# Kernel optimization log

Measured on AMD Instinct MI355X. Metric: run time of the kernel, lower is better.

## Reference

```python
import jax, jax.numpy as jnp
import numpy as np

L, B, T, H = 4, 64, 256, 1024  # layers, batch, seq_len, hidden (=input=output size)


def setup_inputs() -> dict:
    key = jax.random.key(0)
    ks = jax.random.split(key, 5)
    s = 0.03  # ~1/sqrt(H) init scale to avoid gate saturation
    return {
        "x": jax.random.normal(ks[0], (B, T, H), dtype=jnp.float32),
        "W_ih": jax.random.normal(ks[1], (L, 4 * H, H), dtype=jnp.float32) * s,
        "W_hh": jax.random.normal(ks[2], (L, 4 * H, H), dtype=jnp.float32) * s,
        "b_ih": jax.random.normal(ks[3], (L, 4 * H), dtype=jnp.float32) * s,
        "b_hh": jax.random.normal(ks[4], (L, 4 * H), dtype=jnp.float32) * s,
    }


def _lstm_cell(xt, h, c, Wi, Wh, bi, bh):
    # PyTorch LSTMCell: gates = x W_ih^T + b_ih + h W_hh^T + b_hh; order i,f,g,o
    gates = xt @ Wi.T + bi + h @ Wh.T + bh  # [B, 4H]
    i, f, g, o = jnp.split(gates, 4, axis=-1)
    c_new = jax.nn.sigmoid(f) * c + jax.nn.sigmoid(i) * jnp.tanh(g)
    h_new = jax.nn.sigmoid(o) * jnp.tanh(c_new)
    return h_new, c_new


def reference(x, W_ih, W_hh, b_ih, b_hh):
    nlayers, bsz, hid = W_ih.shape[0], x.shape[0], W_hh.shape[-1]
    h0 = jnp.zeros((nlayers, bsz, hid), dtype=x.dtype)
    c0 = jnp.zeros((nlayers, bsz, hid), dtype=x.dtype)

    def step(carry, xt):  # xt: [B, H]
        h, c = carry  # [L, B, H] each
        inp = xt
        hs, cs = [], []
        for l in range(nlayers):  # small fixed layer loop
            h_l, c_l = _lstm_cell(inp, h[l], c[l], W_ih[l], W_hh[l], b_ih[l], b_hh[l])
            hs.append(h_l)
            cs.append(c_l)
            inp = h_l
        return (jnp.stack(hs), jnp.stack(cs)), None

    (h_fin, _), _ = jax.lax.scan(step, (h0, c0), jnp.swapaxes(x, 0, 1))
    return h_fin[-1]  # last layer's hidden at final timestep: [B, output_size]
```

## Files before the change

kernel.cpp:

```cpp
#include <hip/hip_runtime.h>

#define LAYERS 4
#define BATCH  64
#define SEQ    256
#define HID    1024

typedef _Float16 half8 __attribute__((ext_vector_type(8)));
typedef _Float16 half4 __attribute__((ext_vector_type(4)));
typedef float    f32x4 __attribute__((ext_vector_type(4)));
typedef unsigned long long u64;

__device__ __forceinline__ float sig_(float x) { return 1.0f / (1.0f + __expf(-x)); }
__device__ __forceinline__ float th_(float x)  { return 2.0f / (1.0f + __expf(-2.0f * x)) - 1.0f; }

__device__ __forceinline__ void llc_store_h4(_Float16* p, half4 v) {
    union { half4 h; u64 u; } cv; cv.h = v;
    __hip_atomic_store((u64*)p, cv.u, __ATOMIC_RELAXED, __HIP_MEMORY_SCOPE_AGENT);
}

struct BarSt {
    int arrive[LAYERS][16];
    int done[LAYERS][16];
};

__global__ void k_bias(const float* __restrict__ bih, const float* __restrict__ bhh,
                       float* __restrict__ bias) {
    int i = blockIdx.x * blockDim.x + threadIdx.x;
    if (i < LAYERS * 4 * HID) bias[i] = bih[i] + bhh[i];
}

__global__ void k_packw(const float* __restrict__ wih32, const float* __restrict__ whh32,
                        _Float16* __restrict__ wpack) {
    unsigned c = blockIdx.x * blockDim.x + threadIdx.x;
    int lane = c & 63, g = (c >> 6) & 3, il = (c >> 8) & 7, q = (c >> 11) & 3;
    int jblk = (c >> 13) & 63, kh = (c >> 19) & 1, l = (int)(c >> 20);
    const float* src = (kh ? whh32 : wih32)
        + ((size_t)l * 4 * HID + (size_t)g * HID + jblk * 16 + (lane & 15)) * HID
        + (q * 8 + il) * 32 + (lane >> 4) * 8;
    f32x4 a = *(const f32x4*)src;
    f32x4 b = *(const f32x4*)(src + 4);
    half8 d;
    d[0]=(_Float16)a[0]; d[1]=(_Float16)a[1]; d[2]=(_Float16)a[2]; d[3]=(_Float16)a[3];
    d[4]=(_Float16)b[0]; d[5]=(_Float16)b[1]; d[6]=(_Float16)b[2]; d[7]=(_Float16)b[3];
    *(half8*)(wpack + (size_t)c * 8) = d;
}

__global__ void k_packx(const float* __restrict__ x32, _Float16* __restrict__ xpack) {
    unsigned c = blockIdx.x * blockDim.x + threadIdx.x;
    int lane = c & 63, i = (c >> 6) & 31, mt = (c >> 11) & 3, t = (int)(c >> 13);
    int m = mt * 16 + (lane & 15);
    int k = i * 32 + (lane >> 4) * 8;
    const float* src = x32 + ((size_t)m * SEQ + t) * HID + k;
    f32x4 a = *(const f32x4*)src;
    f32x4 b = *(const f32x4*)(src + 4);
    half8 d;
    d[0]=(_Float16)a[0]; d[1]=(_Float16)a[1]; d[2]=(_Float16)a[2]; d[3]=(_Float16)a[3];
    d[4]=(_Float16)b[0]; d[5]=(_Float16)b[1]; d[6]=(_Float16)b[2]; d[7]=(_Float16)b[3];
    *(half8*)(xpack + (size_t)c * 8) = d;
}

__global__ __launch_bounds__(512, 1) void k_persist(
        const _Float16* __restrict__ xpack,
        const _Float16* __restrict__ wpack,
        const float*    __restrict__ bih,
        const float*    __restrict__ bhh,
        _Float16*       __restrict__ hfull,
        BarSt*          __restrict__ bar,
        float*          __restrict__ out)
{
    const int layer = blockIdx.x >> 6;
    const int jblk  = blockIdx.x & 63;
    const int j0    = jblk << 4;
    const int tid   = threadIdx.x;
    const int wave  = tid >> 6;
    const int q     = wave & 3;
    const int kh    = wave >> 2;
    const int lane  = tid & 63;
    const int nl    = lane & 15;
    const int quad  = lane >> 4;
    const size_t BH = (size_t)BATCH * HID;

    __shared__ __align__(16) float gplane[4][4][32][20];
    __shared__ __align__(16) float cbuf[64][16];
    __shared__ __align__(16) float gbias[4][16];

    for (int i = tid; i < 64 * 16; i += 512) ((float*)cbuf)[i] = 0.0f;
    if (tid < 64) {
        int g = tid >> 4, col = tid & 15;
        size_t bidx = (size_t)layer * 4 * HID + (size_t)g * HID + j0 + col;
        gbias[g][col] = bih[bidx] + bhh[bidx];
    }

    const _Float16* Wp = wpack
        + ((((size_t)layer * 2 + kh) * 64 + jblk) * 4 + q) * 16384
        + (size_t)lane * 8;
    half8 wreg[8][4];
    #pragma unroll
    for (int il = 0; il < 8; ++il)
        #pragma unroll
        for (int g = 0; g < 4; ++g)
            wreg[il][g] = *(const half8*)(Wp + il * 2048 + g * 512);

    __syncthreads();

    const bool lastlayer = (layer == LAYERS - 1);

    for (int t = 0; t < SEQ; ++t) {
        if (lane == 0) {
            if (kh == 0) {
                if (layer > 0) {
                    while (__hip_atomic_load(&bar->done[layer - 1][0], __ATOMIC_RELAXED,
                                             __HIP_MEMORY_SCOPE_AGENT) < t + 1)
                        __builtin_amdgcn_s_sleep(1);
                }
            } else {
                if (t > 0) {
                    while (__hip_atomic_load(&bar->done[layer][0], __ATOMIC_RELAXED,
                                             __HIP_MEMORY_SCOPE_AGENT) < t)
                        __builtin_amdgcn_s_sleep(1);
                }
            }
        }
        __builtin_amdgcn_sched_barrier(0);
        asm volatile("" ::: "memory");

        const _Float16* Abase;
        if (kh == 0) {
            Abase = (layer == 0)
                ? (xpack + (size_t)t * BH)
                : (hfull + ((size_t)t * LAYERS + layer) * BH);
        } else {
            Abase = hfull + (t == 0 ? (size_t)0
                                    : ((size_t)(t - 1) * LAYERS + layer + 1)) * BH;
        }
        const _Float16* Ap = Abase + (size_t)q * 4096 + (size_t)lane * 8;

        f32x4 acc[4][4];
        #pragma unroll
        for (int mt = 0; mt < 4; ++mt)
            #pragma unroll
            for (int g = 0; g < 4; ++g) acc[mt][g] = (f32x4){0,0,0,0};

        #pragma unroll
        for (int il = 0; il < 8; ++il) {
            #pragma unroll
            for (int mt = 0; mt < 4; ++mt) {
                half8 a = *(const half8*)(Ap + (size_t)mt * 16384 + il * 512);
                acc[mt][0] = __builtin_amdgcn_mfma_f32_16x16x32_f16(a, wreg[il][0], acc[mt][0], 0,0,0);
                acc[mt][1] = __builtin_amdgcn_mfma_f32_16x16x32_f16(a, wreg[il][1], acc[mt][1], 0,0,0);
                acc[mt][2] = __builtin_amdgcn_mfma_f32_16x16x32_f16(a, wreg[il][2], acc[mt][2], 0,0,0);
                acc[mt][3] = __builtin_amdgcn_mfma_f32_16x16x32_f16(a, wreg[il][3], acc[mt][3], 0,0,0);
            }
        }

        _Float16* hp = hfull + ((size_t)t * LAYERS + layer + 1) * BH;
        const bool last = lastlayer && (t == SEQ - 1);

        #pragma unroll
        for (int half = 0; half < 2; ++half) {
            if (kh == 1) {
                #pragma unroll
                for (int mtl = 0; mtl < 2; ++mtl)
                    #pragma unroll
                    for (int g = 0; g < 4; ++g)
                        #pragma unroll
                        for (int r = 0; r < 4; ++r)
                            gplane[q][g][mtl * 16 + quad * 4 + r][nl] = acc[half * 2 + mtl][g][r];
            }
            __syncthreads();
            if (kh == 0) {
                #pragma unroll
                for (int mtl = 0; mtl < 2; ++mtl)
                    #pragma unroll
                    for (int g = 0; g < 4; ++g)
                        #pragma unroll
                        for (int r = 0; r < 4; ++r)
                            gplane[q][g][mtl * 16 + quad * 4 + r][nl] += acc[half * 2 + mtl][g][r];
            }
            __syncthreads();
            if (tid < 128) {
                const int ml = tid >> 2;
                const int jg = tid & 3;
                const int m  = half * 32 + ml;
                const int jA = j0 + jg * 4;

                f32x4 vi = *(const f32x4*)&gplane[0][0][ml][jg*4] + *(const f32x4*)&gplane[1][0][ml][jg*4]
                         + *(const f32x4*)&gplane[2][0][ml][jg*4] + *(const f32x4*)&gplane[3][0][ml][jg*4];
                f32x4 vf = *(const f32x4*)&gplane[0][1][ml][jg*4] + *(const f32x4*)&gplane[1][1][ml][jg*4]
                         + *(const f32x4*)&gplane[2][1][ml][jg*4] + *(const f32x4*)&gplane[3][1][ml][jg*4];
                f32x4 vg = *(const f32x4*)&gplane[0][2][ml][jg*4] + *(const f32x4*)&gplane[1][2][ml][jg*4]
                         + *(const f32x4*)&gplane[2][2][ml][jg*4] + *(const f32x4*)&gplane[3][2][ml][jg*4];
                f32x4 vo = *(const f32x4*)&gplane[0][3][ml][jg*4] + *(const f32x4*)&gplane[1][3][ml][jg*4]
                         + *(const f32x4*)&gplane[2][3][ml][jg*4] + *(const f32x4*)&gplane[3][3][ml][jg*4];

                f32x4 bi = *(const f32x4*)&gbias[0][jg*4];
                f32x4 bf = *(const f32x4*)&gbias[1][jg*4];
                f32x4 bg = *(const f32x4*)&gbias[2][jg*4];
                f32x4 bo = *(const f32x4*)&gbias[3][jg*4];

                f32x4 c = *(const f32x4*)&cbuf[m][jg*4];
                f32x4 cn, hn;
                #pragma unroll
                for (int i = 0; i < 4; ++i) {
                    float gi = vi[i] + bi[i];
                    float gf = vf[i] + bf[i];
                    float gg = vg[i] + bg[i];
                    float go = vo[i] + bo[i];
                    cn[i] = sig_(gf) * c[i] + sig_(gi) * th_(gg);
                    hn[i] = sig_(go) * th_(cn[i]);
                }
                *(f32x4*)&cbuf[m][jg*4] = cn;

                int i_ = jA >> 5, qd = (jA >> 3) & 3, jj = jA & 7;
                size_t hoff = (size_t)(m >> 4) * 16384 + (size_t)i_ * 512 + qd * 128 + (m & 15) * 8 + jj;
                half4 h4;
                h4[0]=(_Float16)hn[0]; h4[1]=(_Float16)hn[1]; h4[2]=(_Float16)hn[2]; h4[3]=(_Float16)hn[3];
                llc_store_h4(hp + hoff, h4);

                if (last) *(f32x4*)(out + (size_t)m * HID + jA) = hn;
            }
            __syncthreads();
        }

        asm volatile("s_waitcnt vmcnt(0)" ::: "memory");
        __syncthreads();
        if (tid == 0) {
            int a = __hip_atomic_fetch_add(&bar->arrive[layer][0], 1,
                        __ATOMIC_RELAXED, __HIP_MEMORY_SCOPE_AGENT) + 1;
            if (a == 64 * (t + 1))
                __hip_atomic_store(&bar->done[layer][0], t + 1,
                        __ATOMIC_RELAXED, __HIP_MEMORY_SCOPE_AGENT);
        }
    }
}

__global__ __launch_bounds__(512) void k_step(
        int s,
        const _Float16* __restrict__ xpack,
        const _Float16* __restrict__ wpack,
        const float*    __restrict__ bias,
        _Float16*       __restrict__ hbuf,
        float*          __restrict__ cst,
        float*          __restrict__ out)
{
    const int layer = blockIdx.x >> 6;
    const int t = s - layer;
    if (t < 0 || t >= SEQ) return;

    __shared__ __align__(16) float gplane[4][4][32][16];

    const int tid  = threadIdx.x;
    const int wave = tid >> 6;
    const int q    = wave & 3;
    const int kh   = wave >> 2;
    const int lane = tid & 63;
    const int nl   = lane & 15;
    const int quad = lane >> 4;
    const int jblk = blockIdx.x & 63;
    const int j0   = jblk << 4;
    const size_t BH = (size_t)BATCH * HID;

    const _Float16* Abase;
    if (kh == 0) {
        Abase = (layer == 0) ? (xpack + (size_t)t * BH)
                             : (hbuf + ((size_t)(layer - 1) * 2 + (t & 1)) * BH);
    } else {
        Abase = hbuf + ((size_t)layer * 2 + ((t + 1) & 1)) * BH;
    }
    const _Float16* Ap = Abase + (size_t)q * 4096 + (size_t)lane * 8;
    const _Float16* Wp = wpack
        + ((((size_t)layer * 2 + kh) * 64 + jblk) * 4 + q) * 16384
        + (size_t)lane * 8;

    f32x4 acc[4][4];
    #pragma unroll
    for (int mt = 0; mt < 4; ++mt)
        #pragma unroll
        for (int g = 0; g < 4; ++g) acc[mt][g] = (f32x4){0,0,0,0};

    #pragma unroll
    for (int il = 0; il < 8; ++il) {
        half8 w0 = *(const half8*)(Wp + il * 2048 + 0 * 512);
        half8 w1 = *(const half8*)(Wp + il * 2048 + 1 * 512);
        half8 w2 = *(const half8*)(Wp + il * 2048 + 2 * 512);
        half8 w3 = *(const half8*)(Wp + il * 2048 + 3 * 512);
        #pragma unroll
        for (int mt = 0; mt < 4; ++mt) {
            half8 a = *(const half8*)(Ap + (size_t)mt * 16384 + il * 512);
            acc[mt][0] = __builtin_amdgcn_mfma_f32_16x16x32_f16(a, w0, acc[mt][0], 0,0,0);
            acc[mt][1] = __builtin_amdgcn_mfma_f32_16x16x32_f16(a, w1, acc[mt][1], 0,0,0);
            acc[mt][2] = __builtin_amdgcn_mfma_f32_16x16x32_f16(a, w2, acc[mt][2], 0,0,0);
            acc[mt][3] = __builtin_amdgcn_mfma_f32_16x16x32_f16(a, w3, acc[mt][3], 0,0,0);
        }
    }

    const float* bb = bias + (size_t)layer * 4 * HID;
    _Float16* hp = hbuf + ((size_t)layer * 2 + (t & 1)) * BH;
    const bool last = (layer == LAYERS - 1) && (t == SEQ - 1);

    #pragma unroll
    for (int half = 0; half < 2; ++half) {
        if (kh == 1) {
            #pragma unroll
            for (int mtl = 0; mtl < 2; ++mtl)
                #pragma unroll
                for (int g = 0; g < 4; ++g)
                    #pragma unroll
                    for (int r = 0; r < 4; ++r)
                        gplane[q][g][mtl * 16 + quad * 4 + r][nl] = acc[half * 2 + mtl][g][r];
        }
        __syncthreads();
        if (kh == 0) {
            #pragma unroll
            for (int mtl = 0; mtl < 2; ++mtl)
                #pragma unroll
                for (int g = 0; g < 4; ++g)
                    #pragma unroll
                    for (int r = 0; r < 4; ++r)
                        gplane[q][g][mtl * 16 + quad * 4 + r][nl] += acc[half * 2 + mtl][g][r];
        }
        __syncthreads();
        if (tid < 128) {
            const int ml = tid >> 2;
            const int jg = tid & 3;
            const int m  = half * 32 + ml;
            const int jA = j0 + jg * 4;

            f32x4 vi = *(const f32x4*)&gplane[0][0][ml][jg*4] + *(const f32x4*)&gplane[1][0][ml][jg*4]
                     + *(const f32x4*)&gplane[2][0][ml][jg*4] + *(const f32x4*)&gplane[3][0][ml][jg*4];
            f32x4 vf = *(const f32x4*)&gplane[0][1][ml][jg*4] + *(const f32x4*)&gplane[1][1][ml][jg*4]
                     + *(const f32x4*)&gplane[2][1][ml][jg*4] + *(const f32x4*)&gplane[3][1][ml][jg*4];
            f32x4 vg = *(const f32x4*)&gplane[0][2][ml][jg*4] + *(const f32x4*)&gplane[1][2][ml][jg*4]
                     + *(const f32x4*)&gplane[2][2][ml][jg*4] + *(const f32x4*)&gplane[3][2][ml][jg*4];
            f32x4 vo = *(const f32x4*)&gplane[0][3][ml][jg*4] + *(const f32x4*)&gplane[1][3][ml][jg*4]
                     + *(const f32x4*)&gplane[2][3][ml][jg*4] + *(const f32x4*)&gplane[3][3][ml][jg*4];

            f32x4 bi = *(const f32x4*)(bb + 0 * HID + jA);
            f32x4 bf = *(const f32x4*)(bb + 1 * HID + jA);
            f32x4 bg = *(const f32x4*)(bb + 2 * HID + jA);
            f32x4 bo = *(const f32x4*)(bb + 3 * HID + jA);

            float* cp = cst + (size_t)layer * BH + (size_t)m * HID + jA;
            f32x4 c = *(const f32x4*)cp;
            f32x4 cn, hn;
            #pragma unroll
            for (int i = 0; i < 4; ++i) {
                float gi = vi[i] + bi[i];
                float gf = vf[i] + bf[i];
                float gg = vg[i] + bg[i];
                float go = vo[i] + bo[i];
                cn[i] = sig_(gf) * c[i] + sig_(gi) * th_(gg);
                hn[i] = sig_(go) * th_(cn[i]);
            }
            *(f32x4*)cp = cn;

            int i_ = jA >> 5, qd = (jA >> 3) & 3, jj = jA & 7;
            size_t hoff = (size_t)(m >> 4) * 16384 + (size_t)i_ * 512 + qd * 128 + (m & 15) * 8 + jj;
            half4 h4;
            h4[0]=(_Float16)hn[0]; h4[1]=(_Float16)hn[1]; h4[2]=(_Float16)hn[2]; h4[3]=(_Float16)hn[3];
            *(half4*)(hp + hoff) = h4;

            if (last) *(f32x4*)(out + (size_t)m * HID + jA) = hn;
        }
        __syncthreads();
    }
}

extern "C" void kernel_launch(void* const* d_in, const int* in_sizes, int n_in,
                              void* d_out, int out_size, void* d_ws, size_t ws_size,
                              hipStream_t stream) {
    const float* x32   = (const float*)d_in[0];
    const float* wih32 = (const float*)d_in[1];
    const float* whh32 = (const float*)d_in[2];
    const float* bih   = (const float*)d_in[3];
    const float* bhh   = (const float*)d_in[4];
    (void)in_sizes; (void)n_in; (void)out_size;

    const size_t BH = (size_t)BATCH * HID;
    char* ws = (char*)d_ws;
    size_t off = 0;
    _Float16* hpar  = (_Float16*)(ws + off); off += (size_t)LAYERS * 2 * BH * 2;
    float*    cst   = (float*)   (ws + off); off += (size_t)LAYERS * BH * 4;
    BarSt*    bar   = (BarSt*)   (ws + off); off += sizeof(BarSt);
    off = (off + 255) & ~(size_t)255;
    size_t zero_bytes = off;
    float*    bias  = (float*)   (ws + off); off += (size_t)LAYERS * 4 * HID * 4;
    _Float16* wpack = (_Float16*)(ws + off); off += (size_t)2 * LAYERS * 4 * HID * HID * 2;
    _Float16* xpack = (_Float16*)(ws + off); off += (size_t)SEQ * BH * 2;
    _Float16* hfull = (_Float16*)(ws + off);
    size_t full_need = off + (size_t)(SEQ * LAYERS + 1) * BH * 2;
    const int can_persist = (ws_size >= full_need) ? 1 : 0;

    hipMemsetAsync(ws, 0, zero_bytes, stream);
    if (can_persist) hipMemsetAsync(hfull, 0, BH * 2, stream);
    k_bias<<<(LAYERS * 4 * HID + 255) / 256, 256, 0, stream>>>(bih, bhh, bias);
    k_packw<<<(1u << 22) / 256, 256, 0, stream>>>(wih32, whh32, wpack);
    k_packx<<<(1u << 21) / 256, 256, 0, stream>>>(x32, xpack);

    hipError_t cerr = hipErrorUnknown;
    if (can_persist) {
        float* outp = (float*)d_out;
        _Float16* hfull_arg = hfull;
        void* kargs[] = { (void*)&xpack, (void*)&wpack, (void*)&bih, (void*)&bhh,
                          (void*)&hfull_arg, (void*)&bar, (void*)&outp };
        cerr = hipLaunchCooperativeKernel(
            k_persist, dim3(LAYERS * 64), dim3(512), kargs, 0u, stream);
    }

    if (cerr != hipSuccess) {
        for (int s = 0; s < SEQ + LAYERS - 1; ++s)
            k_step<<<LAYERS * 64, 512, 0, stream>>>(
                s, xpack, wpack, bias, hpar, cst, (float*)d_out);
    }
}
```

Measured before the change: 2.855 ms.

## Use hierarchical per-octet barrier and single-pass gate reduction in persistent LSTM

```diff
diff --git a/kernel.cpp b/kernel.cpp
--- a/kernel.cpp
+++ b/kernel.cpp
@@ -19,8 +19,9 @@
 }
 
 struct BarSt {
-    int arrive[LAYERS][16];
-    int done[LAYERS][16];
+    int arrive8[LAYERS][8][16];
+    int rootL[LAYERS][16];
+    int done8[LAYERS][8][16];
 };
 
 __global__ void k_bias(const float* __restrict__ bih, const float* __restrict__ bhh,
@@ -71,6 +72,7 @@
     const int layer = blockIdx.x >> 6;
     const int jblk  = blockIdx.x & 63;
     const int j0    = jblk << 4;
+    const int oct   = jblk >> 3;
     const int tid   = threadIdx.x;
     const int wave  = tid >> 6;
     const int q     = wave & 3;
@@ -80,7 +82,7 @@
     const int quad  = lane >> 4;
     const size_t BH = (size_t)BATCH * HID;
 
-    __shared__ __align__(16) float gplane[4][4][32][20];
+    __shared__ __align__(16) float gplane[2][4][4][32][20];
     __shared__ __align__(16) float cbuf[64][16];
     __shared__ __align__(16) float gbias[4][16];
 
@@ -109,13 +111,13 @@
         if (lane == 0) {
             if (kh == 0) {
                 if (layer > 0) {
-                    while (__hip_atomic_load(&bar->done[layer - 1][0], __ATOMIC_RELAXED,
+                    while (__hip_atomic_load(&bar->done8[layer - 1][oct][0], __ATOMIC_RELAXED,
                                              __HIP_MEMORY_SCOPE_AGENT) < t + 1)
                         __builtin_amdgcn_s_sleep(1);
                 }
             } else {
                 if (t > 0) {
-                    while (__hip_atomic_load(&bar->done[layer][0], __ATOMIC_RELAXED,
+                    while (__hip_atomic_load(&bar->done8[layer][oct][0], __ATOMIC_RELAXED,
                                              __HIP_MEMORY_SCOPE_AGENT) < t)
                         __builtin_amdgcn_s_sleep(1);
                 }
@@ -156,80 +158,88 @@
         _Float16* hp = hfull + ((size_t)t * LAYERS + layer + 1) * BH;
         const bool last = lastlayer && (t == SEQ - 1);
 
-        #pragma unroll
-        for (int half = 0; half < 2; ++half) {
-            if (kh == 1) {
+        if (kh == 1) {
+            #pragma unroll
+            for (int mt = 0; mt < 4; ++mt)
                 #pragma unroll
-                for (int mtl = 0; mtl < 2; ++mtl)
+                for (int g = 0; g < 4; ++g)
                     #pragma unroll
-                    for (int g = 0; g < 4; ++g)
-                        #pragma unroll
-                        for (int r = 0; r < 4; ++r)
-                            gplane[q][g][mtl * 16 + quad * 4 + r][nl] = acc[half * 2 + mtl][g][r];
+                    for (int r = 0; r < 4; ++r) {
+                        int rm = mt * 16 + quad * 4 + r;
+                        gplane[rm >> 5][q][g][rm & 31][nl] = acc[mt][g][r];
+                    }
+        }
+        __syncthreads();
+        if (kh == 0) {
+            #pragma unroll
+            for (int mt = 0; mt < 4; ++mt)
+                #pragma unroll
+                for (int g = 0; g < 4; ++g)
+                    #pragma unroll
+                    for (int r = 0; r < 4; ++r) {
+                        int rm = mt * 16 + quad * 4 + r;
+                        gplane[rm >> 5][q][g][rm & 31][nl] += acc[mt][g][r];
+                    }
+        }
+        __syncthreads();
+        if (tid < 256) {
+            const int m  = tid >> 2;
+            const int hb = m >> 5;
+            const int ml = m & 31;
+            const int jg = tid & 3;
+            const int jA = j0 + jg * 4;
+
+            f32x4 vi = *(const f32x4*)&gplane[hb][0][0][ml][jg*4] + *(const f32x4*)&gplane[hb][1][0][ml][jg*4]
+                     + *(const f32x4*)&gplane[hb][2][0][ml][jg*4] + *(const f32x4*)&gplane[hb][3][0][ml][jg*4];
+            f32x4 vf = *(const f32x4*)&gplane[hb][0][1][ml][jg*4] + *(const f32x4*)&gplane[hb][1][1][ml][jg*4]
+                     + *(const f32x4*)&gplane[hb][2][1][ml][jg*4] + *(const f32x4*)&gplane[hb][3][1][ml][jg*4];
+            f32x4 vg = *(const f32x4*)&gplane[hb][0][2][ml][jg*4] + *(const f32x4*)&gplane[hb][1][2][ml][jg*4]
+                     + *(const f32x4*)&gplane[hb][2][2][ml][jg*4] + *(const f32x4*)&gplane[hb][3][2][ml][jg*4];
+            f32x4 vo = *(const f32x4*)&gplane[hb][0][3][ml][jg*4] + *(const f32x4*)&gplane[hb][1][3][ml][jg*4]
+                     + *(const f32x4*)&gplane[hb][2][3][ml][jg*4] + *(const f32x4*)&gplane[hb][3][3][ml][jg*4];
+
+            f32x4 bi = *(const f32x4*)&gbias[0][jg*4];
+            f32x4 bf = *(const f32x4*)&gbias[1][jg*4];
+            f32x4 bg = *(const f32x4*)&gbias[2][jg*4];
+            f32x4 bo = *(const f32x4*)&gbias[3][jg*4];
+
+            f32x4 c = *(const f32x4*)&cbuf[m][jg*4];
+            f32x4 cn, hn;
+            #pragma unroll
+            for (int i = 0; i < 4; ++i) {
+                float gi = vi[i] + bi[i];
+                float gf = vf[i] + bf[i];
+                float gg = vg[i] + bg[i];
+                float go = vo[i] + bo[i];
+                cn[i] = sig_(gf) * c[i] + sig_(gi) * th_(gg);
+                hn[i] = sig_(go) * th_(cn[i]);
             }
-            __syncthreads();
-            if (kh == 0) {
-                #pragma unroll
-                for (int mtl = 0; mtl < 2; ++mtl)
+            *(f32x4*)&cbuf[m][jg*4] = cn;
+
+            int i_ = jA >> 5, qd = (jA >> 3) & 3, jj = jA & 7;
+            size_t hoff = (size_t)(m >> 4) * 16384 + (size_t)i_ * 512 + qd * 128 + (m & 15) * 8 + jj;
+            half4 h4;
+            h4[0]=(_Float16)hn[0]; h4[1]=(_Float16)hn[1]; h4[2]=(_Float16)hn[2]; h4[3]=(_Float16)hn[3];
+            llc_store_h4(hp + hoff, h4);
+
+            if (last) *(f32x4*)(out + (size_t)m * HID + jA) = hn;
+        }
+
+        asm volatile("s_waitcnt vmcnt(0)" ::: "memory");
+        __syncthreads();
+        if (tid == 0) {
+            int a = __hip_atomic_fetch_add(&bar->arrive8[layer][oct][0], 1,
+                        __ATOMIC_RELAXED, __HIP_MEMORY_SCOPE_AGENT) + 1;
+            if (a == 8 * (t + 1)) {
+                int r = __hip_atomic_fetch_add(&bar->rootL[layer][0], 1,
+                            __ATOMIC_RELAXED, __HIP_MEMORY_SCOPE_AGENT) + 1;
+                if (r == 8 * (t + 1)) {
                     #pragma unroll
-                    for (int g = 0; g < 4; ++g)
-                        #pragma unroll
-                        for (int r = 0; r < 4; ++r)
-                            gplane[q][g][mtl * 16 + quad * 4 + r][nl] += acc[half * 2 + mtl][g][r];
+                    for (int o = 0; o < 8; ++o)
+                        __hip_atomic_store(&bar->done8[layer][o][0], t + 1,
+                                __ATOMIC_RELAXED, __HIP_MEMORY_SCOPE_AGENT);
+                }
             }
-            __syncthreads();
-            if (tid < 128) {
-                const int ml = tid >> 2;
-                const int jg = tid & 3;
-                const int m  = half * 32 + ml;
-                const int jA = j0 + jg * 4;
-
-                f32x4 vi = *(const f32x4*)&gplane[0][0][ml][jg*4] + *(const f32x4*)&gplane[1][0][ml][jg*4]
-                         + *(const f32x4*)&gplane[2][0][ml][jg*4] + *(const f32x4*)&gplane[3][0][ml][jg*4];
-                f32x4 vf = *(const f32x4*)&gplane[0][1][ml][jg*4] + *(const f32x4*)&gplane[1][1][ml][jg*4]
-                         + *(const f32x4*)&gplane[2][1][ml][jg*4] + *(const f32x4*)&gplane[3][1][ml][jg*4];
-                f32x4 vg = *(const f32x4*)&gplane[0][2][ml][jg*4] + *(const f32x4*)&gplane[1][2][ml][jg*4]
-                         + *(const f32x4*)&gplane[2][2][ml][jg*4] + *(const f32x4*)&gplane[3][2][ml][jg*4];
-                f32x4 vo = *(const f32x4*)&gplane[0][3][ml][jg*4] + *(const f32x4*)&gplane[1][3][ml][jg*4]
-                         + *(const f32x4*)&gplane[2][3][ml][jg*4] + *(const f32x4*)&gplane[3][3][ml][jg*4];
-
-                f32x4 bi = *(const f32x4*)&gbias[0][jg*4];
-                f32x4 bf = *(const f32x4*)&gbias[1][jg*4];
-                f32x4 bg = *(const f32x4*)&gbias[2][jg*4];
-                f32x4 bo = *(const f32x4*)&gbias[3][jg*4];
-
-                f32x4 c = *(const f32x4*)&cbuf[m][jg*4];
-                f32x4 cn, hn;
-                #pragma unroll
-                for (int i = 0; i < 4; ++i) {
-                    float gi = vi[i] + bi[i];
-                    float gf = vf[i] + bf[i];
-                    float gg = vg[i] + bg[i];
-                    float go = vo[i] + bo[i];
-                    cn[i] = sig_(gf) * c[i] + sig_(gi) * th_(gg);
-                    hn[i] = sig_(go) * th_(cn[i]);
-                }
-                *(f32x4*)&cbuf[m][jg*4] = cn;
-
-                int i_ = jA >> 5, qd = (jA >> 3) & 3, jj = jA & 7;
-                size_t hoff = (size_t)(m >> 4) * 16384 + (size_t)i_ * 512 + qd * 128 + (m & 15) * 8 + jj;
-                half4 h4;
-                h4[0]=(_Float16)hn[0]; h4[1]=(_Float16)hn[1]; h4[2]=(_Float16)hn[2]; h4[3]=(_Float16)hn[3];
-                llc_store_h4(hp + hoff, h4);
-
-                if (last) *(f32x4*)(out + (size_t)m * HID + jA) = hn;
-            }
-            __syncthreads();
-        }
-
-        asm volatile("s_waitcnt vmcnt(0)" ::: "memory");
-        __syncthreads();
-        if (tid == 0) {
-            int a = __hip_atomic_fetch_add(&bar->arrive[layer][0], 1,
-                        __ATOMIC_RELAXED, __HIP_MEMORY_SCOPE_AGENT) + 1;
-            if (a == 64 * (t + 1))
-                __hip_atomic_store(&bar->done[layer][0], t + 1,
-                        __ATOMIC_RELAXED, __HIP_MEMORY_SCOPE_AGENT);
         }
     }
 }
```

Result: faster. 2.450 ms (-14.2%).
